# Performance work log

Measured on AMD Instinct MI355X. Metric: run time of the kernel, lower is better.

Reference implementation:

```python
import jax, jax.numpy as jnp
import numpy as np
import math

B, C, H, W = 16, 512, 32, 32
HEADS = 8
HD = C // HEADS            # 64 head_dim
NFREQ = HD // 4            # 16 (head_dim % 4 == 0)
MAX_FREQ = 128.0
T = H * W                  # 1024 tokens


def _make_so2_mat():
    # make_2dcoord: meshgrid('ij') of arange(H), arange(W) -> [H, W, 2]
    xg, yg = np.meshgrid(np.arange(H, dtype=np.float32), np.arange(W, dtype=np.float32), indexing='ij')
    coord = np.stack([xg, yg], -1)                                   # [H, W, 2]
    freqs = np.exp(np.linspace(0.0, math.log(MAX_FREQ), NFREQ)).astype(np.float32)  # [NFREQ]
    th = coord[..., None, :] * freqs[None, None, :, None]            # [H, W, NFREQ, 2]
    c, s = np.cos(th), np.sin(th)
    # rotation matrices [[c, -s], [s, c]] -> [H, W, NFREQ, 2(dim), 2, 2]
    mat = np.stack([np.stack([c, -s], -1), np.stack([s, c], -1)], -2)
    mat = mat.reshape(H * W, NFREQ * 2, 2, 2)                        # flatten(2,3) then flatten(0,1)
    return jnp.asarray(mat[:, : HD // 2])                            # [T, HD//2, 2, 2]


def setup_inputs() -> dict:
    key = jax.random.key(0)
    ks = jax.random.split(key, 5)
    mat = _make_so2_mat()
    return {
        'x': jax.random.normal(ks[0], (B, C, H, W), dtype=jnp.float32),
        'w_qkv': jax.random.normal(ks[1], (3 * C, C), dtype=jnp.float32) * 0.02,
        'b_qkv': jax.random.normal(ks[2], (3 * C,), dtype=jnp.float32) * 0.02,
        'w_o': jax.random.normal(ks[3], (C, C), dtype=jnp.float32) * 0.02,
        'b_o': jax.random.normal(ks[4], (C,), dtype=jnp.float32) * 0.02,
        'mat_q': mat,
        'mat_k': mat,
        'mat_v': mat,
        'mat_o': jnp.swapaxes(mat, -2, -1),
    }


def _rep_mul(rep, t):
    # rep: [T, HD//2, 2, 2]; t: [B, nh, T, HD] -> per-pair 2x2 rotation
    tb = t.reshape(B, HEADS, T, HD // 2, 2)
    return jnp.einsum('tfij,bntfj->bntfi', rep, tb).reshape(B, HEADS, T, HD)


def _split_heads(t):
    # 'b (c nh) h w -> b nh (h w) c' (c outer, nh inner in channel dim)
    return t.reshape(B, HD, HEADS, T).transpose(0, 2, 3, 1)


def reference(x, w_qkv, b_qkv, w_o, b_o, mat_q, mat_k, mat_v, mat_o):
    # 1x1 conv QKV projection == channel GEMM
    qkv = jnp.einsum('bchw,oc->bohw', x, w_qkv) + b_qkv[None, :, None, None]
    q, k, v = jnp.split(qkv, 3, axis=1)
    q, k, v = map(_split_heads, (q, k, v))                 # [B, nh, T, HD]
    q = _rep_mul(mat_q, q)
    k = _rep_mul(mat_k, k)
    v = _rep_mul(mat_v, v)
    scale = 1.0 / math.sqrt(HD)
    attn = jax.nn.softmax(jnp.einsum('bntd,bnsd->bnts', q, k) * scale, axis=-1)
    o = jnp.einsum('bnts,bnsd->bntd', attn, v)             # [B, nh, T, HD]
    o = _rep_mul(mat_o, o)
    # 'b nh (h w) c -> b (c nh) h w'
    o = o.reshape(B, HEADS, H, W, HD).transpose(0, 4, 1, 2, 3).reshape(B, C, H, W)
    return jnp.einsum('bchw,oc->bohw', o, w_o) + b_o[None, :, None, None]
```

## Files before the change

### kernel.cpp

```cpp
#include <hip/hip_runtime.h>


typedef __bf16 bf16x8 __attribute__((ext_vector_type(8)));
typedef __bf16 bf16x4 __attribute__((ext_vector_type(4)));
typedef float  f32x4  __attribute__((ext_vector_type(4)));

__device__ __forceinline__ f32x4 mfma16(bf16x8 a, bf16x8 b, f32x4 c) {
    return __builtin_amdgcn_mfma_f32_16x16x32_bf16(a, b, c, 0, 0, 0);
}

__device__ __forceinline__ void async16(const void* g, void* l) {
    __builtin_amdgcn_global_load_lds(
        (const __attribute__((address_space(1))) void*)g,
        (__attribute__((address_space(3))) void*)l, 16, 0, 0);
}

__global__ void k_convert_w(const float* __restrict__ wq, const float* __restrict__ wo,
                            __bf16* __restrict__ wqb, __bf16* __restrict__ wob) {
    int i = blockIdx.x * 256 + threadIdx.x;
    if (i < 3 * 512 * 512) wqb[i] = (__bf16)wq[i];
    if (i < 512 * 512)     wob[i] = (__bf16)wo[i];
}

__global__ void k_transpose_x(const float* __restrict__ x, __bf16* __restrict__ xt) {
    __shared__ float tile[32][33];
    const int b  = blockIdx.z;
    const int c0 = blockIdx.y * 32;
    const int t0 = blockIdx.x * 32;
    const int tx = threadIdx.x, ty = threadIdx.y;
    const float* xp = x + ((size_t)b * 512 + c0) * 1024 + t0;
#pragma unroll
    for (int j = 0; j < 4; j++)
        tile[ty + j * 8][tx] = xp[(ty + j * 8) * 1024 + tx];
    __syncthreads();
    __bf16* xo = xt + ((size_t)b * 1024 + t0) * 512 + c0;
#pragma unroll
    for (int j = 0; j < 4; j++)
        xo[(ty + j * 8) * 512 + tx] = (__bf16)tile[tx][ty + j * 8];
}

__global__ __launch_bounds__(256) void k_gemm_qkv(
        const __bf16* __restrict__ A, const __bf16* __restrict__ W,
        const float* __restrict__ bias,
        const float* __restrict__ matq, const float* __restrict__ matk,
        const float* __restrict__ matv,
        __bf16* __restrict__ qd, __bf16* __restrict__ kd, __bf16* __restrict__ vtd)
{
    __shared__ __bf16 As[128][64];
    __shared__ __bf16 Bs[128][64];
    const int tid = threadIdx.x;
    const int m0 = blockIdx.x * 128;
    const int jb = blockIdx.y;
    const int part = jb >> 2;
    const int nh_base = (jb & 3) * 2;
    const int lane = tid & 63, w = tid >> 6;
    const int ln = lane & 15, quad = lane >> 4;
    const int wr = w >> 1, wc = w & 1;

    const int srow = lane >> 3;
    const int scol = (((lane & 7) ^ srow) * 8);

    const __bf16* arow[4];
    const __bf16* brow[4];
#pragma unroll
    for (int jj = 0; jj < 4; jj++) {
        int rr = w * 32 + jj * 8 + srow;
        arow[jj] = &A[(size_t)(m0 + rr) * 512 + scol];
        int o = part * 512 + (rr & 63) * 8 + nh_base + (rr >> 6);
        brow[jj] = &W[(size_t)o * 512 + scol];
    }

    f32x4 acc[4][4] = {};

    for (int k0 = 0; k0 < 512; k0 += 64) {
#pragma unroll
        for (int jj = 0; jj < 4; jj++)
            async16(arow[jj] + k0, &As[w * 32 + jj * 8][0]);
#pragma unroll
        for (int jj = 0; jj < 4; jj++)
            async16(brow[jj] + k0, &Bs[w * 32 + jj * 8][0]);
        __syncthreads();
#pragma unroll
        for (int h = 0; h < 2; h++) {
            bf16x8 af[4], wf[4];
#pragma unroll
            for (int mi = 0; mi < 4; mi++)
                af[mi] = *(const bf16x8*)&As[wr * 64 + mi * 16 + ln][(((h * 4 + quad) ^ (ln & 7)) * 8)];
#pragma unroll
            for (int ni = 0; ni < 4; ni++)
                wf[ni] = *(const bf16x8*)&Bs[wc * 64 + ni * 16 + ln][(((h * 4 + quad) ^ (ln & 7)) * 8)];
#pragma unroll
            for (int mi = 0; mi < 4; mi++)
#pragma unroll
                for (int ni = 0; ni < 4; ni++)
                    acc[mi][ni] = mfma16(af[mi], wf[ni], acc[mi][ni]);
        }
        __syncthreads();
    }

    const int nh = nh_base + wc;
    const int rowbase = m0 + wr * 64;
    const int b  = rowbase >> 10, t0 = rowbase & 1023;
    const int bh = b * 8 + nh;
    const int ip = ln & 1;
    const float2* matp = (const float2*)(part == 0 ? matq : (part == 1 ? matk : matv));
    __bf16* qkdst = (part == 0) ? qd : kd;

#pragma unroll
    for (int ni = 0; ni < 4; ni++) {
        const int hd = ni * 16 + ln;
        const int f  = hd >> 1;
        const float bias_o = bias[part * 512 + hd * 8 + nh];
#pragma unroll
        for (int mi = 0; mi < 4; mi++) {
            const int tq = t0 + mi * 16 + quad * 4;
            if (part < 2) {
#pragma unroll
                for (int r = 0; r < 4; r++) {
                    int t = tq + r;
                    float val = acc[mi][ni][r] + bias_o;
                    float pr  = __shfl_xor(val, 1);
                    float2 mv = matp[((size_t)t * 32 + f) * 2 + ip];
                    float e  = ip ? pr : val;
                    float oo = ip ? val : pr;
                    float rv = mv.x * e + mv.y * oo;
                    qkdst[((size_t)bh * 1024 + t) * 64 + hd] = (__bf16)rv;
                }
            } else {
                __bf16 pack[4];
#pragma unroll
                for (int r = 0; r < 4; r++) {
                    int t = tq + r;
                    float val = acc[mi][ni][r] + bias_o;
                    float pr  = __shfl_xor(val, 1);
                    float2 mv = matp[((size_t)t * 32 + f) * 2 + ip];
                    float e  = ip ? pr : val;
                    float oo = ip ? val : pr;
                    pack[r] = (__bf16)(mv.x * e + mv.y * oo);
                }
                *(uint2*)&vtd[((size_t)bh * 64 + hd) * 1024 + tq] = *(const uint2*)pack;
            }
        }
    }
}

__global__ __launch_bounds__(256) void k_attn(
        const __bf16* __restrict__ q, const __bf16* __restrict__ kk,
        const __bf16* __restrict__ vt, const float* __restrict__ mato,
        __bf16* __restrict__ od)
{
    __shared__ __bf16 Ks[64][64];
    __shared__ __bf16 Vs[64][64];
    __shared__ __bf16 Ps[4][32][64];
    const int bh = blockIdx.x, qt = blockIdx.y;
    const int b = bh >> 3;
    const int tid = threadIdx.x, w = tid >> 6, lane = tid & 63;
    const int ln = lane & 15, quad = lane >> 4;
    const int lx = ln & 7;
    const int srow = lane >> 3;
    const int scol = ((lane & 7) ^ srow) * 8;
    const int qr0 = qt * 128 + w * 32;

    bf16x8 qa[2][2];
#pragma unroll
    for (int mi = 0; mi < 2; mi++)
#pragma unroll
        for (int ki = 0; ki < 2; ki++)
            qa[mi][ki] = *(const bf16x8*)&q[((size_t)bh * 1024 + qr0 + mi * 16 + ln) * 64 + ki * 32 + quad * 8];

    const __bf16* kbase = kk + (size_t)bh * 1024 * 64;
    const __bf16* vbase = vt + (size_t)bh * 64 * 1024;

    f32x4 oacc[2][4] = {};
    f32x4 lacc[2] = {};
    const float C_EXP = 0.18033688011112042f;

    bf16x8 ones;
#pragma unroll
    for (int j = 0; j < 8; j++) ones[j] = (__bf16)1.0f;

    for (int st = 0; st < 16; st++) {
#pragma unroll
        for (int i = 0; i < 2; i++) {
            int r0 = w * 16 + i * 8;
            async16(kbase + (size_t)(st * 64 + r0 + srow) * 64 + scol, &Ks[r0][0]);
            async16(vbase + (size_t)(r0 + srow) * 1024 + st * 64 + scol, &Vs[r0][0]);
        }
        __syncthreads();

#pragma unroll
        for (int si = 0; si < 4; si++) {
            bf16x8 kb0 = *(const bf16x8*)&Ks[si * 16 + ln][((quad    ) ^ lx) * 8];
            bf16x8 kb1 = *(const bf16x8*)&Ks[si * 16 + ln][((quad + 4) ^ lx) * 8];
            f32x4 sc[2] = {};
#pragma unroll
            for (int mi = 0; mi < 2; mi++) {
                sc[mi] = mfma16(kb0, qa[mi][0], sc[mi]);
                sc[mi] = mfma16(kb1, qa[mi][1], sc[mi]);
            }
#pragma unroll
            for (int mi = 0; mi < 2; mi++) {
                bf16x4 pk;
#pragma unroll
                for (int r = 0; r < 4; r++)
                    pk[r] = (__bf16)exp2f(sc[mi][r] * C_EXP);
                *(bf16x4*)((char*)&Ps[w][mi * 16 + ln][0]
                           + (((si * 2 + (quad >> 1)) ^ lx) * 16) + (quad & 1) * 8) = pk;
            }
        }

#pragma unroll
        for (int kt = 0; kt < 2; kt++) {
            bf16x8 pa[2];
#pragma unroll
            for (int mi = 0; mi < 2; mi++)
                pa[mi] = *(const bf16x8*)&Ps[w][mi * 16 + ln][((kt * 4 + quad) ^ lx) * 8];
#pragma unroll
            for (int ni = 0; ni < 4; ni++) {
                bf16x8 vb = *(const bf16x8*)&Vs[ni * 16 + ln][((kt * 4 + quad) ^ lx) * 8];
                oacc[0][ni] = mfma16(pa[0], vb, oacc[0][ni]);
                oacc[1][ni] = mfma16(pa[1], vb, oacc[1][ni]);
            }
            lacc[0] = mfma16(pa[0], ones, lacc[0]);
            lacc[1] = mfma16(pa[1], ones, lacc[1]);
        }
        __syncthreads();
    }

    float inv[2][4];
#pragma unroll
    for (int mi = 0; mi < 2; mi++)
#pragma unroll
        for (int r = 0; r < 4; r++)
            inv[mi][r] = 1.0f / lacc[mi][r];

    const int nh = bh & 7;
    const float2* mo2 = (const float2*)mato;
#pragma unroll
    for (int mi = 0; mi < 2; mi++) {
#pragma unroll
        for (int ni = 0; ni < 4; ni++) {
            int hd = ni * 16 + ln;
            int f = hd >> 1, ip = ln & 1;
#pragma unroll
            for (int r = 0; r < 4; r++) {
                int t = qr0 + mi * 16 + quad * 4 + r;
                float val = oacc[mi][ni][r] * inv[mi][r];
                float pr  = __shfl_xor(val, 1);
                float2 mv = mo2[(t * 32 + f) * 2 + ip];
                float e  = ip ? pr : val;
                float oo = ip ? val : pr;
                float rv = mv.x * e + mv.y * oo;
                od[((size_t)b * 1024 + t) * 512 + hd * 8 + nh] = (__bf16)rv;
            }
        }
    }
}

__global__ __launch_bounds__(256) void k_gemm_out(
        const __bf16* __restrict__ A, const __bf16* __restrict__ W,
        const float* __restrict__ bias, float* __restrict__ out)
{
    __shared__ __bf16 As[128][64];
    __shared__ __bf16 Bs[128][64];
    const int tid = threadIdx.x;
    const int m0 = blockIdx.x * 128;
    const int n0 = blockIdx.y * 128;
    const int lane = tid & 63, w = tid >> 6;
    const int ln = lane & 15, quad = lane >> 4;
    const int wr = w >> 1, wc = w & 1;

    const int srow = lane >> 3;
    const int scol = (((lane & 7) ^ srow) * 8);

    const __bf16* arow[4];
    const __bf16* brow[4];
#pragma unroll
    for (int jj = 0; jj < 4; jj++) {
        int rr = w * 32 + jj * 8 + srow;
        arow[jj] = &A[(size_t)(m0 + rr) * 512 + scol];
        brow[jj] = &W[(size_t)(n0 + rr) * 512 + scol];
    }

    f32x4 acc[4][4] = {};

    for (int k0 = 0; k0 < 512; k0 += 64) {
#pragma unroll
        for (int jj = 0; jj < 4; jj++)
            async16(arow[jj] + k0, &As[w * 32 + jj * 8][0]);
#pragma unroll
        for (int jj = 0; jj < 4; jj++)
            async16(brow[jj] + k0, &Bs[w * 32 + jj * 8][0]);
        __syncthreads();
#pragma unroll
        for (int h = 0; h < 2; h++) {
            bf16x8 af[4], wf[4];
#pragma unroll
            for (int mi = 0; mi < 4; mi++)
                af[mi] = *(const bf16x8*)&As[wr * 64 + mi * 16 + ln][(((h * 4 + quad) ^ (ln & 7)) * 8)];
#pragma unroll
            for (int ni = 0; ni < 4; ni++)
                wf[ni] = *(const bf16x8*)&Bs[wc * 64 + ni * 16 + ln][(((h * 4 + quad) ^ (ln & 7)) * 8)];
#pragma unroll
            for (int mi = 0; mi < 4; mi++)
#pragma unroll
                for (int ni = 0; ni < 4; ni++)
                    acc[mi][ni] = mfma16(af[mi], wf[ni], acc[mi][ni]);
        }
        __syncthreads();
    }

    const int rowbase = m0 + wr * 64;
    const int bb = rowbase >> 10, t0 = rowbase & 1023;
#pragma unroll
    for (int ni = 0; ni < 4; ni++) {
        int o = n0 + wc * 64 + ni * 16 + ln;
        float bias_o = bias[o];
#pragma unroll
        for (int mi = 0; mi < 4; mi++) {
            int t = t0 + mi * 16 + quad * 4;
            f32x4 v = acc[mi][ni];
            v[0] += bias_o; v[1] += bias_o; v[2] += bias_o; v[3] += bias_o;
            *(f32x4*)&out[((size_t)bb * 512 + o) * 1024 + t] = v;
        }
    }
}

extern "C" void kernel_launch(void* const* d_in, const int* in_sizes, int n_in,
                              void* d_out, int out_size, void* d_ws, size_t ws_size,
                              hipStream_t stream) {
    (void)in_sizes; (void)n_in; (void)out_size; (void)ws_size;
    const float* x     = (const float*)d_in[0];
    const float* w_qkv = (const float*)d_in[1];
    const float* b_qkv = (const float*)d_in[2];
    const float* w_o   = (const float*)d_in[3];
    const float* b_o   = (const float*)d_in[4];
    const float* mat_q = (const float*)d_in[5];
    const float* mat_k = (const float*)d_in[6];
    const float* mat_v = (const float*)d_in[7];
    const float* mat_o = (const float*)d_in[8];
    float* out = (float*)d_out;

    char* p = (char*)d_ws;
    __bf16* wqb = (__bf16*)p;  p += (size_t)3 * 512 * 512 * 2;
    __bf16* wob = (__bf16*)p;  p += (size_t)512 * 512 * 2;
    char* xt_base = p;
    __bf16* xt  = (__bf16*)p;  p += (size_t)16384 * 512 * 2;
    __bf16* qd  = (__bf16*)p;  p += (size_t)128 * 1024 * 64 * 2;
    __bf16* kd  = (__bf16*)p;  p += (size_t)128 * 1024 * 64 * 2;
    __bf16* vtd = (__bf16*)p;  p += (size_t)128 * 64 * 1024 * 2;
    __bf16* od  = (__bf16*)xt_base;

    k_convert_w  <<<dim3(3072),       dim3(256),    0, stream>>>(w_qkv, w_o, wqb, wob);
    k_transpose_x<<<dim3(32, 16, 16), dim3(32, 8),  0, stream>>>(x, xt);
    k_gemm_qkv   <<<dim3(128, 12),    dim3(256),    0, stream>>>(xt, wqb, b_qkv, mat_q, mat_k, mat_v, qd, kd, vtd);
    k_attn       <<<dim3(128, 8),     dim3(256),    0, stream>>>(qd, kd, vtd, mat_o, od);
    k_gemm_out   <<<dim3(128, 4),     dim3(256),    0, stream>>>(od, wob, b_o, out);
}
```

Baseline: 250.1 us.

## Store attention output head-major with vector writes and permute w_o columns to match

The attention epilogue swaps the MFMA operands so each lane holds four consecutive head-dim values for a single token. It then applies the output rotation with float4 matrix loads and writes 8-byte packed bf16 values into a [B, heads, T, 64] layout. Previously it used shuffles and scattered 2-byte stores strided by the head count. To compensate, the output-projection weights are permuted at conversion time and the output GEMM reads A along the head-major layout. This is meant to remove the uncoalesced scattered stores, at the cost of more strided A-tile loads in the GEMM.

Measured after the change: 240.8 us. 1.04x faster.

```diff
diff --git a/kernel.cpp b/kernel.cpp
--- a/kernel.cpp
+++ b/kernel.cpp
@@ -19,7 +19,11 @@
                             __bf16* __restrict__ wqb, __bf16* __restrict__ wob) {
     int i = blockIdx.x * 256 + threadIdx.x;
     if (i < 3 * 512 * 512) wqb[i] = (__bf16)wq[i];
-    if (i < 512 * 512)     wob[i] = (__bf16)wo[i];
+    if (i < 512 * 512) {
+        int o = i >> 9, k2 = i & 511;
+        int nh = k2 >> 6, hd = k2 & 63;
+        wob[i] = (__bf16)wo[o * 512 + hd * 8 + nh];
+    }
 }
 
 __global__ void k_transpose_x(const float* __restrict__ x, __bf16* __restrict__ xt) {
@@ -153,7 +157,6 @@
     __shared__ __bf16 Vs[64][64];
     __shared__ __bf16 Ps[4][32][64];
     const int bh = blockIdx.x, qt = blockIdx.y;
-    const int b = bh >> 3;
     const int tid = threadIdx.x, w = tid >> 6, lane = tid & 63;
     const int ln = lane & 15, quad = lane >> 4;
     const int lx = ln & 7;
@@ -218,41 +221,36 @@
 #pragma unroll
             for (int ni = 0; ni < 4; ni++) {
                 bf16x8 vb = *(const bf16x8*)&Vs[ni * 16 + ln][((kt * 4 + quad) ^ lx) * 8];
-                oacc[0][ni] = mfma16(pa[0], vb, oacc[0][ni]);
-                oacc[1][ni] = mfma16(pa[1], vb, oacc[1][ni]);
+                oacc[0][ni] = mfma16(vb, pa[0], oacc[0][ni]);
+                oacc[1][ni] = mfma16(vb, pa[1], oacc[1][ni]);
             }
-            lacc[0] = mfma16(pa[0], ones, lacc[0]);
-            lacc[1] = mfma16(pa[1], ones, lacc[1]);
-        }
-        __syncthreads();
-    }
-
-    float inv[2][4];
-#pragma unroll
-    for (int mi = 0; mi < 2; mi++)
-#pragma unroll
-        for (int r = 0; r < 4; r++)
-            inv[mi][r] = 1.0f / lacc[mi][r];
-
-    const int nh = bh & 7;
-    const float2* mo2 = (const float2*)mato;
+            lacc[0] = mfma16(ones, pa[0], lacc[0]);
+            lacc[1] = mfma16(ones, pa[1], lacc[1]);
+        }
+        __syncthreads();
+    }
+
+    const float4* mo4 = (const float4*)mato;
 #pragma unroll
     for (int mi = 0; mi < 2; mi++) {
+        const int t = qr0 + mi * 16 + ln;
+        const float invl = 1.0f / lacc[mi][0];
 #pragma unroll
         for (int ni = 0; ni < 4; ni++) {
-            int hd = ni * 16 + ln;
-            int f = hd >> 1, ip = ln & 1;
-#pragma unroll
-            for (int r = 0; r < 4; r++) {
-                int t = qr0 + mi * 16 + quad * 4 + r;
-                float val = oacc[mi][ni][r] * inv[mi][r];
-                float pr  = __shfl_xor(val, 1);
-                float2 mv = mo2[(t * 32 + f) * 2 + ip];
-                float e  = ip ? pr : val;
-                float oo = ip ? val : pr;
-                float rv = mv.x * e + mv.y * oo;
-                od[((size_t)b * 1024 + t) * 512 + hd * 8 + nh] = (__bf16)rv;
-            }
+            const int hd0 = ni * 16 + quad * 4;
+            const int f   = hd0 >> 1;
+            float v0 = oacc[mi][ni][0] * invl;
+            float v1 = oacc[mi][ni][1] * invl;
+            float v2 = oacc[mi][ni][2] * invl;
+            float v3 = oacc[mi][ni][3] * invl;
+            float4 m1 = mo4[(size_t)t * 32 + f];
+            float4 m2 = mo4[(size_t)t * 32 + f + 1];
+            __bf16 pk[4];
+            pk[0] = (__bf16)(m1.x * v0 + m1.y * v1);
+            pk[1] = (__bf16)(m1.z * v0 + m1.w * v1);
+            pk[2] = (__bf16)(m2.x * v2 + m2.y * v3);
+            pk[3] = (__bf16)(m2.z * v2 + m2.w * v3);
+            *(uint2*)&od[((size_t)bh * 1024 + t) * 64 + hd0] = *(const uint2*)pk;
         }
     }
 }
@@ -273,12 +271,14 @@
     const int srow = lane >> 3;
     const int scol = (((lane & 7) ^ srow) * 8);
 
+    const int bb = m0 >> 10, t00 = m0 & 1023;
+
     const __bf16* arow[4];
     const __bf16* brow[4];
 #pragma unroll
     for (int jj = 0; jj < 4; jj++) {
         int rr = w * 32 + jj * 8 + srow;
-        arow[jj] = &A[(size_t)(m0 + rr) * 512 + scol];
+        arow[jj] = &A[((size_t)bb * 8192 + t00 + rr) * 64 + scol];
         brow[jj] = &W[(size_t)(n0 + rr) * 512 + scol];
     }
 
@@ -287,7 +287,7 @@
     for (int k0 = 0; k0 < 512; k0 += 64) {
 #pragma unroll
         for (int jj = 0; jj < 4; jj++)
-            async16(arow[jj] + k0, &As[w * 32 + jj * 8][0]);
+            async16(arow[jj] + (size_t)k0 * 1024, &As[w * 32 + jj * 8][0]);
 #pragma unroll
         for (int jj = 0; jj < 4; jj++)
             async16(brow[jj] + k0, &Bs[w * 32 + jj * 8][0]);
@@ -311,7 +311,7 @@
     }
 
     const int rowbase = m0 + wr * 64;
-    const int bb = rowbase >> 10, t0 = rowbase & 1023;
+    const int bb2 = rowbase >> 10, t0 = rowbase & 1023;
 #pragma unroll
     for (int ni = 0; ni < 4; ni++) {
         int o = n0 + wc * 64 + ni * 16 + ln;
@@ -321,7 +321,7 @@
             int t = t0 + mi * 16 + quad * 4;
             f32x4 v = acc[mi][ni];
             v[0] += bias_o; v[1] += bias_o; v[2] += bias_o; v[3] += bias_o;
-            *(f32x4*)&out[((size_t)bb * 512 + o) * 1024 + t] = v;
+            *(f32x4*)&out[((size_t)bb2 * 512 + o) * 1024 + t] = v;
         }
     }
 }
```
